# Kernel optimization log

Hardware: AMD Instinct MI355X
Metric: run time of the kernel (lower is better)

## Reference

```python
import jax, jax.numpy as jnp
import numpy as np

UNITS = 128
INPUT_SIZE = 64
BATCH = 2048
SDE_UNFOLDS = 6
ODE_UNFOLDS = 6


def setup_inputs() -> dict:
    key = jax.random.key(0)
    ks = jax.random.split(key, 16)
    U, I, B = UNITS, INPUT_SIZE, BATCH
    inp = {
        "inputs": jax.random.normal(ks[0], (B, I), dtype=jnp.float32),
        "states": jax.random.normal(ks[1], (B, U), dtype=jnp.float32),
        "input_weights": jnp.ones((I,), dtype=jnp.float32),
        "input_biases": jnp.zeros((I,), dtype=jnp.float32),
        "sensory_mu": jax.random.uniform(ks[2], (I, U), minval=0.3, maxval=0.8, dtype=jnp.float32),
        "sensory_sigma": jax.random.uniform(ks[3], (I, U), minval=3.0, maxval=8.0, dtype=jnp.float32),
        "sensory_W": jax.random.uniform(ks[4], (I, U), minval=0.01, maxval=1.0, dtype=jnp.float32),
        "sensory_erev": (2.0 * jax.random.randint(ks[5], (I, U), 0, 2).astype(jnp.float32) - 1.0),
        "mu": jax.random.uniform(ks[6], (U, U), minval=0.3, maxval=0.8, dtype=jnp.float32),
        "sigma": jax.random.uniform(ks[7], (U, U), minval=3.0, maxval=8.0, dtype=jnp.float32),
        "W": jax.random.uniform(ks[8], (U, U), minval=0.01, maxval=1.0, dtype=jnp.float32),
        "erev": (2.0 * jax.random.randint(ks[9], (U, U), 0, 2).astype(jnp.float32) - 1.0),
        "vleak": jax.random.uniform(ks[10], (U,), minval=-0.2, maxval=0.2, dtype=jnp.float32),
        "gleak": jnp.ones((U,), dtype=jnp.float32),   # gleak_init_min == gleak_init_max == 1
        "cm_t": jnp.full((U,), 0.5, dtype=jnp.float32),  # cm_init_min == cm_init_max == 0.5
    }
    return inp


def _syn_sigmoid(v, mu, sigma):
    # v: [B, D]; mu, sigma: [D, U] -> [B, D, U]
    return jax.nn.sigmoid(sigma * (v[:, :, None] - mu))


def reference(inputs, states, input_weights, input_biases,
              sensory_mu, sensory_sigma, sensory_W, sensory_erev,
              mu, sigma, W, erev, vleak, gleak, cm_t):
    # affine input mapping
    x = inputs * input_weights + input_biases  # [B, I]

    # sensory synaptic activation (constant across unfolds, compute once)
    sens_act = sensory_W * _syn_sigmoid(x, sensory_mu, sensory_sigma)  # [B, I, U]
    w_num_s = jnp.sum(sens_act * sensory_erev, axis=1)  # [B, U]
    w_den_s = jnp.sum(sens_act, axis=1)                 # [B, U]

    def drift(v):
        # inner LTC fused ODE solver (6 unfolds)
        for _ in range(ODE_UNFOLDS):
            w_act = W * _syn_sigmoid(v, mu, sigma)      # [B, U, U]
            w_num = jnp.sum(w_act * erev, axis=1) + w_num_s
            w_den = jnp.sum(w_act, axis=1) + w_den_s
            v = (cm_t * v + gleak * vleak + w_num) / (cm_t + gleak + w_den)
        return v

    # Euler-Maruyama outer loop; diffusion term is unimplemented (None) in the
    # source, treated as zero, so states += drift * time_step (time_step = 1)
    s = states
    for _ in range(SDE_UNFOLDS):
        s = s + drift(s)
    return s
```

## Files before the change

kernel.cpp:

```cpp
#include <hip/hip_runtime.h>


#define LOG2E 1.4426950408889634f

constexpr int U   = 128;
constexpr int I   = 64;
constexpr int B   = 2048;
constexpr int M   = 4;
constexpr int S   = 4;
constexpr int BLK = U * S;
constexpr int RPT = U / S;
constexpr int SDE = 6, ODE = 6;

#if __has_builtin(__builtin_amdgcn_exp2f)
#define EXP2(x) __builtin_amdgcn_exp2f(x)
#else
#define EXP2(x) exp2f(x)
#endif
#if __has_builtin(__builtin_amdgcn_rcpf)
#define RCP(x) __builtin_amdgcn_rcpf(x)
#else
#define RCP(x) (1.0f / (x))
#endif

#define SIGACC(P, V, PN, PD)                                   \
  {                                                            \
    float t_ = fmaf((P).x, (V), (P).y);                        \
    float e_ = EXP2(t_);                                       \
    float r_ = RCP(1.0f + e_);                                 \
    (PN) = fmaf((P).z, r_, (PN));                              \
    (PD) = fmaf((P).w, r_, (PD));                              \
  }

__global__ __launch_bounds__(256) void pack_params(
    const float* __restrict__ mu, const float* __restrict__ sigma,
    const float* __restrict__ W, const float* __restrict__ erev,
    const float* __restrict__ smu, const float* __restrict__ ssig,
    const float* __restrict__ sW, const float* __restrict__ serev,
    float4* __restrict__ pp, float4* __restrict__ ps)
{
  int idx = blockIdx.x * 256 + threadIdx.x;
  if (idx < U * U) {
    float sg = sigma[idx];
    float w  = W[idx];
    pp[idx] = make_float4(-LOG2E * sg, LOG2E * sg * mu[idx], w * erev[idx], w);
  } else if (idx < U * U + I * U) {
    int k = idx - U * U;
    float sg = ssig[k];
    float w  = sW[k];
    ps[k] = make_float4(-LOG2E * sg, LOG2E * sg * smu[k], w * serev[k], w);
  }
}

__global__ __launch_bounds__(BLK, 2) void ltc_kernel(
    const float4* __restrict__ pp, const float4* __restrict__ ps,
    const float* __restrict__ inputs, const float* __restrict__ states,
    const float* __restrict__ iw, const float* __restrict__ ibias,
    const float* __restrict__ vleak, const float* __restrict__ gleak,
    const float* __restrict__ cmt, float* __restrict__ out)
{
  __shared__ __align__(16) float v_lds[M][U];
  __shared__ __align__(16) float x_lds[M][I];
  __shared__ float2 part[S][M][U];

  const int tid = threadIdx.x;
  const int j   = tid & (U - 1);
  const int s   = tid >> 7;
  const int b0  = blockIdx.x * M;

  const float cm = cmt[j];
  const float gl = gleak[j];
  const float gv = gl * vleak[j];
  const float cg = cm + gl;

  float4 P[RPT];
#pragma unroll
  for (int k = 0; k < RPT; ++k) P[k] = pp[(s * RPT + k) * U + j];

  if (tid < M * I) {
    const int m = tid >> 6, i = tid & (I - 1);
    x_lds[m][i] = inputs[(b0 + m) * I + i] * iw[i] + ibias[i];
  }
  __syncthreads();

  float wns[M], wds[M];
  {
    float pn[M], pd[M];
#pragma unroll
    for (int m = 0; m < M; ++m) { pn[m] = 0.f; pd[m] = 0.f; }
#pragma unroll
    for (int ii = 0; ii < I / S; ii += 4) {
      const int i = s * (I / S) + ii;
      const float4 p0 = ps[(i + 0) * U + j];
      const float4 p1 = ps[(i + 1) * U + j];
      const float4 p2 = ps[(i + 2) * U + j];
      const float4 p3 = ps[(i + 3) * U + j];
#pragma unroll
      for (int m = 0; m < M; ++m) {
        const float4 xv = *reinterpret_cast<const float4*>(&x_lds[m][i]);
        SIGACC(p0, xv.x, pn[m], pd[m]);
        SIGACC(p1, xv.y, pn[m], pd[m]);
        SIGACC(p2, xv.z, pn[m], pd[m]);
        SIGACC(p3, xv.w, pn[m], pd[m]);
      }
    }
#pragma unroll
    for (int m = 0; m < M; ++m) part[s][m][j] = make_float2(pn[m], pd[m]);
    __syncthreads();
#pragma unroll
    for (int m = 0; m < M; ++m) {
      float n = 0.f, d = 0.f;
#pragma unroll
      for (int t2 = 0; t2 < S; ++t2) { const float2 f = part[t2][m][j]; n += f.x; d += f.y; }
      wns[m] = n; wds[m] = d;
    }
  }

  float sv[M];
#pragma unroll
  for (int m = 0; m < M; ++m) sv[m] = states[(b0 + m) * U + j];

  float vj[M];
  for (int sde = 0; sde < SDE; ++sde) {
#pragma unroll
    for (int m = 0; m < M; ++m) vj[m] = sv[m];
    if (s == 0) {
#pragma unroll
      for (int m = 0; m < M; ++m) v_lds[m][j] = sv[m];
    }
    __syncthreads();

    for (int ode = 0; ode < ODE; ++ode) {
      float pn[M], pd[M];
#pragma unroll
      for (int m = 0; m < M; ++m) { pn[m] = 0.f; pd[m] = 0.f; }
#pragma unroll
      for (int kk = 0; kk < RPT; kk += 4) {
        const int i = s * RPT + kk;
#pragma unroll
        for (int m = 0; m < M; ++m) {
          const float4 vv = *reinterpret_cast<const float4*>(&v_lds[m][i]);
          SIGACC(P[kk + 0], vv.x, pn[m], pd[m]);
          SIGACC(P[kk + 1], vv.y, pn[m], pd[m]);
          SIGACC(P[kk + 2], vv.z, pn[m], pd[m]);
          SIGACC(P[kk + 3], vv.w, pn[m], pd[m]);
        }
      }
#pragma unroll
      for (int m = 0; m < M; ++m) part[s][m][j] = make_float2(pn[m], pd[m]);
      __syncthreads();
#pragma unroll
      for (int m = 0; m < M; ++m) {
        float n = wns[m], d = wds[m];
#pragma unroll
        for (int t2 = 0; t2 < S; ++t2) { const float2 f = part[t2][m][j]; n += f.x; d += f.y; }
        const float den = cg + d;
        float r = RCP(den);
        r = r * (2.0f - den * r);
        vj[m] = (fmaf(cm, vj[m], gv) + n) * r;
      }
      if (s == 0) {
#pragma unroll
        for (int m = 0; m < M; ++m) v_lds[m][j] = vj[m];
      }
      __syncthreads();
    }
#pragma unroll
    for (int m = 0; m < M; ++m) sv[m] += vj[m];
  }

  if (s == 0) {
#pragma unroll
    for (int m = 0; m < M; ++m) out[(b0 + m) * U + j] = sv[m];
  }
}

extern "C" void kernel_launch(void* const* d_in, const int* in_sizes, int n_in,
                              void* d_out, int out_size, void* d_ws, size_t ws_size,
                              hipStream_t stream) {
  const float* inputs = (const float*)d_in[0];
  const float* states = (const float*)d_in[1];
  const float* iw     = (const float*)d_in[2];
  const float* ibias  = (const float*)d_in[3];
  const float* smu    = (const float*)d_in[4];
  const float* ssig   = (const float*)d_in[5];
  const float* sW     = (const float*)d_in[6];
  const float* serev  = (const float*)d_in[7];
  const float* mu     = (const float*)d_in[8];
  const float* sigma  = (const float*)d_in[9];
  const float* W      = (const float*)d_in[10];
  const float* erev   = (const float*)d_in[11];
  const float* vleak  = (const float*)d_in[12];
  const float* gleak  = (const float*)d_in[13];
  const float* cmt    = (const float*)d_in[14];
  float* out = (float*)d_out;

  float4* pp = (float4*)d_ws;
  float4* ps = pp + U * U;

  const int packN = U * U + I * U;
  pack_params<<<(packN + 255) / 256, 256, 0, stream>>>(
      mu, sigma, W, erev, smu, ssig, sW, serev, pp, ps);
  ltc_kernel<<<B / M, BLK, 0, stream>>>(
      pp, ps, inputs, states, iw, ibias, vleak, gleak, cmt, out);
}
```

Before: 358.7 us.

## Reduce partial sums with wave shuffles and double-buffer state to drop barriers

Remaps threads so the four K-slices for a given output unit sit in the same 64-lane wavefront, then reduces the partial numerator and denominator with xor shuffles instead of an LDS partial array. This removes one __syncthreads per ODE step. The voltage vector is double-buffered in LDS so each step needs only a single barrier. It also pins the parameter registers with an empty asm and switches to waves_per_eu(2,2). The cost is that the s==0 lanes are now spread across every wave, and shuffle latency replaces the LDS round trip.

```diff
diff --git a/kernel.cpp b/kernel.cpp
--- a/kernel.cpp
+++ b/kernel.cpp
@@ -8,7 +8,7 @@
 constexpr int B   = 2048;
 constexpr int M   = 4;
 constexpr int S   = 4;
-constexpr int BLK = U * S;
+constexpr int BLK = 512;
 constexpr int RPT = U / S;
 constexpr int SDE = 6, ODE = 6;
 
@@ -52,20 +52,22 @@
   }
 }
 
-__global__ __launch_bounds__(BLK, 2) void ltc_kernel(
+__global__ __launch_bounds__(BLK)
+__attribute__((amdgpu_waves_per_eu(2, 2)))
+void ltc_kernel(
     const float4* __restrict__ pp, const float4* __restrict__ ps,
     const float* __restrict__ inputs, const float* __restrict__ states,
     const float* __restrict__ iw, const float* __restrict__ ibias,
     const float* __restrict__ vleak, const float* __restrict__ gleak,
     const float* __restrict__ cmt, float* __restrict__ out)
 {
-  __shared__ __align__(16) float v_lds[M][U];
+  __shared__ __align__(16) float4 v4[2][M][U / 4];
   __shared__ __align__(16) float x_lds[M][I];
-  __shared__ float2 part[S][M][U];
 
   const int tid = threadIdx.x;
-  const int j   = tid & (U - 1);
-  const int s   = tid >> 7;
+  const int jlo = tid & 15;
+  const int s   = (tid >> 4) & 3;
+  const int j   = ((tid >> 6) << 4) | jlo;
   const int b0  = blockIdx.x * M;
 
   const float cm = cmt[j];
@@ -89,8 +91,8 @@
 #pragma unroll
     for (int m = 0; m < M; ++m) { pn[m] = 0.f; pd[m] = 0.f; }
 #pragma unroll
-    for (int ii = 0; ii < I / S; ii += 4) {
-      const int i = s * (I / S) + ii;
+    for (int q = 0; q < 4; ++q) {
+      const int i = s * 16 + q * 4;
       const float4 p0 = ps[(i + 0) * U + j];
       const float4 p1 = ps[(i + 1) * U + j];
       const float4 p2 = ps[(i + 2) * U + j];
@@ -105,28 +107,32 @@
       }
     }
 #pragma unroll
-    for (int m = 0; m < M; ++m) part[s][m][j] = make_float2(pn[m], pd[m]);
-    __syncthreads();
-#pragma unroll
     for (int m = 0; m < M; ++m) {
-      float n = 0.f, d = 0.f;
-#pragma unroll
-      for (int t2 = 0; t2 < S; ++t2) { const float2 f = part[t2][m][j]; n += f.x; d += f.y; }
+      float n = pn[m], d = pd[m];
+      n += __shfl_xor(n, 16); n += __shfl_xor(n, 32);
+      d += __shfl_xor(d, 16); d += __shfl_xor(d, 32);
       wns[m] = n; wds[m] = d;
     }
   }
 
+#pragma unroll
+  for (int k = 0; k < RPT; ++k)
+    asm volatile("" : "+v"(P[k].x), "+v"(P[k].y), "+v"(P[k].z), "+v"(P[k].w));
+
   float sv[M];
 #pragma unroll
   for (int m = 0; m < M; ++m) sv[m] = states[(b0 + m) * U + j];
 
+  int buf = 0;
   float vj[M];
   for (int sde = 0; sde < SDE; ++sde) {
 #pragma unroll
     for (int m = 0; m < M; ++m) vj[m] = sv[m];
+    buf ^= 1;
     if (s == 0) {
 #pragma unroll
-      for (int m = 0; m < M; ++m) v_lds[m][j] = sv[m];
+      for (int m = 0; m < M; ++m)
+        reinterpret_cast<float*>(&v4[buf][m][0])[j] = sv[m];
     }
     __syncthreads();
 
@@ -135,33 +141,32 @@
 #pragma unroll
       for (int m = 0; m < M; ++m) { pn[m] = 0.f; pd[m] = 0.f; }
 #pragma unroll
-      for (int kk = 0; kk < RPT; kk += 4) {
-        const int i = s * RPT + kk;
+      for (int q = 0; q < 8; ++q) {
 #pragma unroll
         for (int m = 0; m < M; ++m) {
-          const float4 vv = *reinterpret_cast<const float4*>(&v_lds[m][i]);
-          SIGACC(P[kk + 0], vv.x, pn[m], pd[m]);
-          SIGACC(P[kk + 1], vv.y, pn[m], pd[m]);
-          SIGACC(P[kk + 2], vv.z, pn[m], pd[m]);
-          SIGACC(P[kk + 3], vv.w, pn[m], pd[m]);
+          const float4 vv = v4[buf][m][s * 8 + q];
+          SIGACC(P[q * 4 + 0], vv.x, pn[m], pd[m]);
+          SIGACC(P[q * 4 + 1], vv.y, pn[m], pd[m]);
+          SIGACC(P[q * 4 + 2], vv.z, pn[m], pd[m]);
+          SIGACC(P[q * 4 + 3], vv.w, pn[m], pd[m]);
         }
       }
 #pragma unroll
-      for (int m = 0; m < M; ++m) part[s][m][j] = make_float2(pn[m], pd[m]);
-      __syncthreads();
-#pragma unroll
       for (int m = 0; m < M; ++m) {
-        float n = wns[m], d = wds[m];
-#pragma unroll
-        for (int t2 = 0; t2 < S; ++t2) { const float2 f = part[t2][m][j]; n += f.x; d += f.y; }
+        float n = pn[m], d = pd[m];
+        n += __shfl_xor(n, 16); n += __shfl_xor(n, 32);
+        d += __shfl_xor(d, 16); d += __shfl_xor(d, 32);
+        n += wns[m]; d += wds[m];
         const float den = cg + d;
         float r = RCP(den);
         r = r * (2.0f - den * r);
         vj[m] = (fmaf(cm, vj[m], gv) + n) * r;
       }
+      buf ^= 1;
       if (s == 0) {
 #pragma unroll
-        for (int m = 0; m < M; ++m) v_lds[m][j] = vj[m];
+        for (int m = 0; m < M; ++m)
+          reinterpret_cast<float*>(&v4[buf][m][0])[j] = vj[m];
       }
       __syncthreads();
     }
```

Result: slower. 415.6 us (+15.8%).
